# Performance work log

Hardware: AMD Instinct MI355X
Metric: run time of the kernel (lower is better)

Reference implementation:

```python
import jax, jax.numpy as jnp
import numpy as np

N, DZ, DQ = 65536, 128, 512


def setup_inputs() -> dict:
    key = jax.random.key(0)
    kz, kb, kg = jax.random.split(key, 3)
    z = jax.random.normal(kz, (N, DZ), dtype=jnp.float32)
    # match torch init scaling: beta ~ 0.01*randn, gamma ~ 0.05*randn
    beta = jax.random.normal(kb, (DQ, DZ), dtype=jnp.float32) * 0.01
    gamma = jax.random.normal(kg, (DQ, DZ), dtype=jnp.float32) * 0.05
    return {"z": z, "beta": beta, "gamma": gamma}


def reference(z, beta, gamma):
    # zero-inflated Poisson sampling decoder
    logits = jnp.einsum("nd,qd->nq", z, beta)          # [N, dq]
    pi = jax.nn.sigmoid(logits)                          # exp(x)/(1+exp(x))
    rate = jnp.nan_to_num(jnp.exp(jnp.einsum("nd,qd->nq", z, gamma)), nan=1e-4)
    rate = jnp.abs(rate) + 0.01
    key = jax.random.key(42)
    kp, kb = jax.random.split(key)
    poisson = jax.random.poisson(kp, rate).astype(jnp.float32)   # [N, dq]
    masking = jax.random.bernoulli(kb, 1.0 - pi).astype(jnp.float32)
    return masking * poisson
```

## Files before the change

### kernel.cpp

```cpp
#include <hip/hip_runtime.h>
#include <stdint.h>

#pragma clang fp contract(off)

#define HALF_ 16777216u

#define WS_TSLOT 386
#define WS_RCNT  388
#define WS_P1E5  392
#define TBL_OFF_B 4096
#define TBL_K0 95904
#define TBL_N  8193
#define RWL_OFF_B   81920
#define RWLCAP 16384u
#define PCNT_OFF_B  212992
#define KCNT_OFF_B  475136
#define BTT_OFF_B   786432
#define GTT_OFF_B   1048576
#define DYN2_OFF_B  1310720
#define PCAP_BLK 128u
#define KCAP_BLK 128u
#define NBLK 65536u
#define P1WL_OFF_B  DYN2_OFF_B
#define KWL_OFF_B   (DYN2_OFF_B + 33554432u)
#define NEED_V4     (KWL_OFF_B + 33554432u)
#define V2WL_OFF_B 40960
#define V2WLCAP 16384u
#define V2BT_OFF_B 172032

__device__ __forceinline__ void tf2x32(uint32_t k0, uint32_t k1,
                                       uint32_t x0, uint32_t x1,
                                       uint32_t& o0, uint32_t& o1) {
  uint32_t ks2 = k0 ^ k1 ^ 0x1BD11BDAu;
  x0 += k0; x1 += k1;
#define TFR(r) x0 += x1; x1 = (x1 << (r)) | (x1 >> (32 - (r))); x1 ^= x0;
  TFR(13) TFR(15) TFR(26) TFR(6)
  x0 += k1;  x1 += ks2 + 1u;
  TFR(17) TFR(29) TFR(16) TFR(24)
  x0 += ks2; x1 += k0 + 2u;
  TFR(13) TFR(15) TFR(26) TFR(6)
  x0 += k0;  x1 += k1 + 3u;
  TFR(17) TFR(29) TFR(16) TFR(24)
  x0 += k1;  x1 += ks2 + 4u;
  TFR(13) TFR(15) TFR(26) TFR(6)
  x0 += ks2; x1 += k0 + 5u;
#undef TFR
  o0 = x0; o1 = x1;
}

__device__ __forceinline__ uint32_t tfx(uint32_t k0, uint32_t k1, uint32_t i) {
  uint32_t o0, o1;
  tf2x32(k0, k1, 0u, i, o0, o1);
  return o0 ^ o1;
}

__device__ __forceinline__ float u01(uint32_t bits) {
  return __uint_as_float((bits >> 9) | 0x3f800000u) - 1.0f;
}

__device__ __forceinline__ float csqrt(float x) {
  return (float)__builtin_sqrt((double)x);
}

__device__ __forceinline__ float eexp(float xin) {
  float c = fminf(xin, 88.3762626647950f);
  c = fmaxf(c, -88.3762626647949f);
  float fx = floorf(__builtin_fmaf(c, 1.44269504088896341f, 0.5f));
  float x = __builtin_fmaf(-0.693359375f, fx, c);
  x = __builtin_fmaf(2.12194440e-4f, fx, x);
  float z = x * x;
  float y = __builtin_fmaf(x, 1.9875691500e-4f, 1.3981999507e-3f);
  y = __builtin_fmaf(y, x, 8.3334519073e-3f);
  y = __builtin_fmaf(y, x, 4.1665795894e-2f);
  y = __builtin_fmaf(y, x, 1.6666665459e-1f);
  y = __builtin_fmaf(y, x, 5.0000001201e-1f);
  y = __builtin_fmaf(y, z, x);
  y = 1.0f + y;
  int e = (int)fx;
  float s = __uint_as_float((uint32_t)(e + 127) << 23);
  return fmaxf(y * s, xin);
}

__device__ __forceinline__ float elog(float xin) {
  float x = fmaxf(xin, 1.17549435e-38f);
  uint32_t bits = __float_as_uint(x);
  float e = (float)((int)(bits >> 23) - 0x7e);
  x = __uint_as_float((bits & 0x807fffffu) | 0x3f000000u);
  bool mask = x < 0.707106781186547524f;
  float tmp = mask ? x : 0.0f;
  x = x - 1.0f;
  e = e - (mask ? 1.0f : 0.0f);
  x = x + tmp;
  float z = x * x;
  float y = __builtin_fmaf(7.0376836292e-2f, x, -1.1514610310e-1f);
  y = __builtin_fmaf(y, x, 1.1676998740e-1f);
  y = __builtin_fmaf(y, x, -1.2420140846e-1f);
  y = __builtin_fmaf(y, x, 1.4249322787e-1f);
  y = __builtin_fmaf(y, x, -1.6668057665e-1f);
  y = __builtin_fmaf(y, x, 2.0000714765e-1f);
  y = __builtin_fmaf(y, x, -2.4999993993e-1f);
  y = __builtin_fmaf(y, x, 3.3333331174e-1f);
  y = y * x;
  y = y * z;
  y = __builtin_fmaf(e, -2.12194440e-4f, y);
  y = __builtin_fmaf(-0.5f, z, y);
  x = x + y;
  x = __builtin_fmaf(e, 0.693359375f, x);
  if (xin == 0.0f) x = -__builtin_inff();
  return x;
}

__device__ __forceinline__ float xlog1p(float x) {
  float small_ = __builtin_fmaf(-0.5f, x, 1.0f) * x;
  float large_ = elog(x + 1.0f);
  return (fabsf(x) < 1e-4f) ? small_ : large_;
}

__device__ __forceinline__ float xlgamma(float input) {
  float z = input - 1.0f;
  float x = 0.99999999999980993227684700473478f;
  const float lcs[8] = {
      676.520368121885098567009190444019f,
      -1259.13921672240287047156078755283f,
      771.3234287776530788486528258894f,
      -176.61502916214059906584551354f,
      12.507343278686904814458936853f,
      -0.13857109526572011689554707f,
      9.984369578019570859563e-6f,
      1.50563273514931155834e-7f};
#pragma unroll
  for (int i = 0; i < 8; ++i) {
    x = x + lcs[i] / ((z + (float)i) + 1.0f);
  }
  float t = 7.5f + z;
  float log_t = 2.0149030205422647f + xlog1p(z / 7.5f);
  float log_y = __builtin_fmaf((z + 0.5f) - t / log_t, log_t,
                               0.91893853320467274178f) + elog(x);
  return log_y;
}

struct TrsP { float ll, bb, aa, ia, vr; };
__device__ __forceinline__ TrsP trs_params(float lam) {
  TrsP p;
  p.ll = elog(lam);
  p.bb = __builtin_fmaf(2.53f, csqrt(lam), 0.931f);
  p.aa = __builtin_fmaf(0.02483f, p.bb, -0.059f);
  p.ia = 1.1239f + 1.1328f / (p.bb - 3.4f);
  p.vr = 0.9277f - 3.6224f / (p.bb - 2.0f);
  return p;
}

__device__ __forceinline__ bool trs_step(float lam, const TrsP& p,
                                         float u, float v, float& kout) {
  float us = 0.5f - fabsf(u);
  float t2 = (2.0f * p.aa) / us + p.bb;
  float k = floorf(__builtin_fmaf(t2, u, lam) + 0.43f);
  kout = k;
  bool accept1 = (us >= 0.07f) && (v <= p.vr);
  if (accept1) return true;
  bool reject = (k < 0.0f) || ((us < 0.013f) && (v > us));
  if (reject) return false;
  float s = elog(v * p.ia / (p.aa / (us * us) + p.bb));
  float tt = __builtin_fmaf(k, p.ll, -lam) - xlgamma(k + 1.0f);
  return s <= tt;
}

__global__ void chain_v2(uint32_t* __restrict__ ws) {
  int lane = threadIdx.x;
  uint32_t kpa = 0, kpb = 0;
  if (lane == 0) {
    uint32_t a0, b0;
    tf2x32(0u, 42u, 0u, 0u, kpa, kpb);
    tf2x32(0u, 42u, 0u, 1u, a0, b0);
    ws[0] = a0; ws[1] = b0;
  }
  kpa = __shfl(kpa, 0); kpb = __shfl(kpb, 0);
  uint32_t kra = kpa, krb = kpb;
  uint32_t kja = kpa, kjb = kpb;
  for (int i = 0; i < 64; ++i) {
    bool isrej = (lane >= 2 && lane <= 4);
    uint32_t key0 = isrej ? kja : kra;
    uint32_t key1 = isrej ? kjb : krb;
    uint32_t xx = (lane == 1) ? 1u : (lane == 3) ? 1u : (lane == 4) ? 2u : 0u;
    uint32_t o0, o1;
    tf2x32(key0, key1, 0u, xx, o0, o1);
    if (lane == 1) { ws[2 + 2 * i] = o0; ws[3 + 2 * i] = o1; }
    if (lane == 3) { ws[130 + 4 * i] = o0; ws[131 + 4 * i] = o1; }
    if (lane == 4) { ws[132 + 4 * i] = o0; ws[133 + 4 * i] = o1; }
    kra = __shfl(o0, 0); krb = __shfl(o1, 0);
    kja = __shfl(o0, 2); kjb = __shfl(o1, 2);
  }
  if (lane == 0) {
    TrsP p = trs_params(1e5f);
    float* wf = (float*)(ws + WS_P1E5);
    wf[0] = p.ll; wf[1] = p.bb; wf[2] = p.aa; wf[3] = p.ia; wf[4] = p.vr;
    ws[WS_TSLOT] = 0u;
    ws[WS_RCNT] = 0u;
  }
}

__global__ __launch_bounds__(256) void lgt_kernel(uint32_t* __restrict__ ws) {
  int j = blockIdx.x * 256 + threadIdx.x;
  if (j >= TBL_N) return;
  float* tbl = (float*)((char*)ws + TBL_OFF_B);
  tbl[j] = xlgamma((float)(TBL_K0 + j) + 1.0f);
}

__global__ __launch_bounds__(256) void transpose_kernel(
    const float* __restrict__ b, const float* __restrict__ g,
    float* __restrict__ bT, float* __restrict__ gT) {
  int i = blockIdx.x * 256 + threadIdx.x;
  int q = i >> 7, d = i & 127;
  bT[d * 512 + q] = b[i];
  gT[d * 512 + q] = g[i];
}

__global__ __launch_bounds__(256) void transpose_tiled(
    const float* __restrict__ b, const float* __restrict__ g,
    float* __restrict__ bTT, float* __restrict__ gTT) {
  int i = blockIdx.x * 256 + threadIdx.x;
  int q = i >> 7, d = i & 127;
  int dst = (d >> 2) * 2048 + (q << 2) + (d & 3);
  bTT[dst] = b[i];
  gTT[dst] = g[i];
}

struct P1C { float ll, bb, aa, ia, vr; };

__device__ __forceinline__ bool p1_eval(const P1C& c, const float* __restrict__ tbl,
                                        uint32_t s00, uint32_t s01,
                                        uint32_t s10, uint32_t s11, uint32_t idx) {
  float u = u01(tfx(s00, s01, idx)) - 0.5f;
  float v = u01(tfx(s10, s11, idx));
  float us = 0.5f - fabsf(u);
  if (us >= 0.07f && v <= c.vr) return true;
  float t2 = (2.0f * c.aa) / us + c.bb;
  float k = floorf(__builtin_fmaf(t2, u, 1e5f) + 0.43f);
  if ((k < 0.0f) || ((us < 0.013f) && (v > us))) return false;
  float arg = v * c.ia / (c.aa / (us * us) + c.bb);
  int ki = (int)k - TBL_K0;
  float lg = (ki >= 0 && ki < TBL_N) ? tbl[ki] : xlgamma(k + 1.0f);
  float tt = __builtin_fmaf(k, c.ll, -1e5f) - lg;
  float sf = __logf(arg);
  if (sf <= tt - 1e-4f) return true;
  if (sf > tt + 1e-4f) return false;
  return elog(arg) <= tt;
}

__device__ uint32_t p1_scan(const P1C& c, const float* __restrict__ tbl,
                            const uint32_t* __restrict__ rej, uint32_t idx) {
  for (int it = 1; it < 64; ++it) {
    if (p1_eval(c, tbl, rej[4 * it], rej[4 * it + 1], rej[4 * it + 2],
                rej[4 * it + 3], idx))
      return (uint32_t)it;
  }
  return 63u;
}

__global__ __launch_bounds__(256) void p1a_v4(
    uint32_t* ws, uint32_t* __restrict__ p1wl, uint32_t* __restrict__ pcnt) {
  __shared__ uint32_t ldsc;
  if (threadIdx.x == 0) ldsc = 0;
  __syncthreads();
  const float* wf = (const float*)(ws + WS_P1E5);
  P1C c{wf[0], wf[1], wf[2], wf[3], wf[4]};
  const float* tbl = (const float*)((const char*)ws + TBL_OFF_B);
  const uint32_t* rej = ws + 130;
  uint32_t s00 = rej[0], s01 = rej[1], s10 = rej[2], s11 = rej[3];
  uint32_t t = blockIdx.x * 256u + threadIdx.x;
  uint32_t* region = p1wl + blockIdx.x * PCAP_BLK;
  bool fa = !p1_eval(c, tbl, s00, s01, s10, s11, t);
  bool fb = !p1_eval(c, tbl, s00, s01, s10, s11, t + HALF_);
  if (fa) {
    uint32_t slot = atomicAdd(&ldsc, 1u);
    if (slot < PCAP_BLK) region[slot] = t;
    else atomicMax(ws + WS_TSLOT, p1_scan(c, tbl, rej, t));
  }
  if (fb) {
    uint32_t slot = atomicAdd(&ldsc, 1u);
    if (slot < PCAP_BLK) region[slot] = t + HALF_;
    else atomicMax(ws + WS_TSLOT, p1_scan(c, tbl, rej, t + HALF_));
  }
  __syncthreads();
  if (threadIdx.x == 0) pcnt[blockIdx.x] = ldsc;
}

__global__ __launch_bounds__(256) void p1b_v4(
    uint32_t* ws, const uint32_t* __restrict__ p1wl,
    const uint32_t* __restrict__ pcnt) {
  const float* wf = (const float*)(ws + WS_P1E5);
  P1C c{wf[0], wf[1], wf[2], wf[3], wf[4]};
  const float* tbl = (const float*)((const char*)ws + TBL_OFF_B);
  const uint32_t* rej = ws + 130;
  uint32_t fmax = 0;
  uint32_t total = NBLK * PCAP_BLK;
  for (uint32_t s = blockIdx.x * 256u + threadIdx.x; s < total;
       s += gridDim.x * 256u) {
    uint32_t b = s >> 7, i = s & (PCAP_BLK - 1u);
    uint32_t cnt = pcnt[b];
    if (cnt > PCAP_BLK) cnt = PCAP_BLK;
    if (i < cnt) {
      uint32_t f = p1_scan(c, tbl, rej, p1wl[s]);
      if (f > fmax) fmax = f;
    }
  }
  for (int off = 32; off > 0; off >>= 1) {
    uint32_t o = __shfl_down(fmax, off, 64);
    if (o > fmax) fmax = o;
  }
  if ((threadIdx.x & 63) == 0 && fmax > 0) atomicMax(ws + WS_TSLOT, fmax);
}

__device__ __forceinline__ int first_accept_exact(float lam, uint32_t idx,
                                                  const uint32_t* __restrict__ rej) {
  TrsP p = trs_params(lam);
  for (int it = 0; it < 64; ++it) {
    float u = u01(tfx(rej[4 * it + 0], rej[4 * it + 1], idx)) - 0.5f;
    float v = u01(tfx(rej[4 * it + 2], rej[4 * it + 3], idx));
    float kk;
    if (trs_step(lam, p, u, v, kk)) return it;
  }
  return 63;
}

__device__ float knuth_finish(float lp, float lam, bool fD, bool m,
                              const uint32_t* __restrict__ wsk, uint32_t idx) {
  const float del = 4e-6f * (lam + 4.0f);
  int k = 4;
  bool fU = false;
  for (int it = 4; it < 64; ++it) {
    float d = lp + lam;
    bool nb = fabsf(d) < del;
    if (d > 0.0f) {
      fD = nb; k++;
      lp = lp + __logf(u01(tfx(wsk[2 * it], wsk[2 * it + 1], idx)));
    } else { fU = nb; break; }
  }
  float p = (float)(k - 1);
  float ph = p + ((fD && fU) ? 0.0f : (fD ? -0.5f : (fU ? 0.5f : 0.0f)));
  return m ? ph : 0.0f;
}

__global__ __launch_bounds__(256) void zip_v4(
    const float* __restrict__ z, uint32_t* ws,
    uint32_t* __restrict__ kwl, uint32_t* __restrict__ kcnt,
    float* __restrict__ out) {
  __shared__ uint32_t ldsc;
  if (threadIdx.x == 0) ldsc = 0;
  __syncthreads();
  uint32_t t = blockIdx.x * 256u + threadIdx.x;
  uint32_t n = t >> 9, q = t & 511u, n2 = n + 32768u;

  const float4* z4a = (const float4*)(z + (size_t)n * 128u);
  const float4* z4b = (const float4*)(z + (size_t)n2 * 128u);
  const float4* bt4 = (const float4*)((const char*)ws + BTT_OFF_B);
  const float4* gt4 = (const float4*)((const char*)ws + GTT_OFF_B);

  float lA = 0.f, lB = 0.f, gA = 0.f, gB = 0.f;
  for (int d4 = 0; d4 < 32; ++d4) {
    float4 bv = bt4[(d4 << 9) + q];
    float4 gv = gt4[(d4 << 9) + q];
    float4 z1 = z4a[d4], z2 = z4b[d4];
    lA = lA + z1.x * bv.x; lB = lB + z2.x * bv.x; gA = gA + z1.x * gv.x; gB = gB + z2.x * gv.x;
    lA = lA + z1.y * bv.y; lB = lB + z2.y * bv.y; gA = gA + z1.y * gv.y; gB = gB + z2.y * gv.y;
    lA = lA + z1.z * bv.z; lB = lB + z2.z * bv.z; gA = gA + z1.z * gv.z; gB = gB + z2.z * gv.z;
    lA = lA + z1.w * bv.w; lB = lB + z2.w * bv.w; gA = gA + z1.w * gv.w; gB = gB + z2.w * gv.w;
  }

  float piA = 1.0f / (1.0f + eexp(-lA));
  float piB = 1.0f / (1.0f + eexp(-lB));
  float lamA = fabsf(eexp(gA)) + 0.01f;
  float lamB = fabsf(eexp(gB)) + 0.01f;

  float dmA = u01(tfx(ws[0], ws[1], t)) - (1.0f - piA);
  float dmB = u01(tfx(ws[0], ws[1], t + HALF_)) - (1.0f - piB);
  bool mA = dmA < 0.0f, mB = dmB < 0.0f;
  bool mfA = fabsf(dmA) < 2e-6f, mfB = fabsf(dmB) < 2e-6f;

  bool knuA = lamA < 10.0f, knuB = lamB < 10.0f;

  const uint32_t* wsk = ws + 2;
  const float delA = 4e-6f * (lamA + 4.0f);
  const float delB = 4e-6f * (lamB + 4.0f);
  float lpA = 0.f, lpB = 0.f;
  int kA = 0, kB = 0;
  bool goA = knuA, goB = knuB;
  bool fDA = false, fUA = false, fDB = false, fUB = false;
#pragma unroll
  for (int it = 0; it < 4; ++it) {
    uint32_t w0 = wsk[2 * it], w1 = wsk[2 * it + 1];
    if (goA) {
      float d = lpA + lamA;
      bool nb = fabsf(d) < delA;
      if (d > 0.0f) { fDA = nb; kA++; lpA = lpA + __logf(u01(tfx(w0, w1, t))); }
      else          { fUA = nb; goA = false; }
    }
    if (goB) {
      float d = lpB + lamB;
      bool nb = fabsf(d) < delB;
      if (d > 0.0f) { fDB = nb; kB++; lpB = lpB + __logf(u01(tfx(w0, w1, t + HALF_))); }
      else          { fUB = nb; goB = false; }
    }
  }
  bool survA = knuA && goA, survB = knuB && goB;

  const uint32_t* rejk = ws + 130;
  uint32_t* rwl = (uint32_t*)((char*)ws + RWL_OFF_B);
  if (!knuA) {
    atomicMax(ws + WS_TSLOT, (uint32_t)first_accept_exact(lamA, t, rejk));
    uint32_t slot = atomicAdd(ws + WS_RCNT, 1u);
    if (slot < RWLCAP) {
      rwl[2 * slot] = t | (mA ? 0x80000000u : 0u);
      rwl[2 * slot + 1] = __float_as_uint(lamA);
    }
  }
  if (!knuB) {
    atomicMax(ws + WS_TSLOT, (uint32_t)first_accept_exact(lamB, t + HALF_, rejk));
    uint32_t slot = atomicAdd(ws + WS_RCNT, 1u);
    if (slot < RWLCAP) {
      rwl[2 * slot] = (t + HALF_) | (mB ? 0x80000000u : 0u);
      rwl[2 * slot + 1] = __float_as_uint(lamB);
    }
  }

  uint32_t* region = kwl + blockIdx.x * KCAP_BLK;
  if (survA) {
    uint32_t slot = atomicAdd(&ldsc, 1u);
    if (slot < KCAP_BLK) region[slot] = t | ((uint32_t)mA << 25);
    else out[t] = knuth_finish(lpA, lamA, fDA, mA, wsk, t);
  } else if (knuA) {
    float pA = (float)(kA - 1);
    float hiA = pA + (fUA ? 0.5f : 0.0f);
    float resA;
    if (mfA && hiA <= 1.2f) resA = 0.5f * hiA;
    else {
      float ph = pA + ((fDA && fUA) ? 0.0f : (fDA ? -0.5f : (fUA ? 0.5f : 0.0f)));
      resA = mA ? ph : 0.0f;
    }
    out[t] = resA;
  } else {
    out[t] = 0.0f;
  }

  if (survB) {
    uint32_t slot = atomicAdd(&ldsc, 1u);
    if (slot < KCAP_BLK) region[slot] = (t + HALF_) | ((uint32_t)mB << 25);
    else out[t + HALF_] = knuth_finish(lpB, lamB, fDB, mB, wsk, t + HALF_);
  } else if (knuB) {
    float pB = (float)(kB - 1);
    float hiB = pB + (fUB ? 0.5f : 0.0f);
    float resB;
    if (mfB && hiB <= 1.2f) resB = 0.5f * hiB;
    else {
      float ph = pB + ((fDB && fUB) ? 0.0f : (fDB ? -0.5f : (fUB ? 0.5f : 0.0f)));
      resB = mB ? ph : 0.0f;
    }
    out[t + HALF_] = resB;
  } else {
    out[t + HALF_] = 0.0f;
  }
  __syncthreads();
  if (threadIdx.x == 0) kcnt[blockIdx.x] = ldsc;
}

__global__ __launch_bounds__(256) void k3b_v4(
    uint32_t* ws, const float* __restrict__ z,
    const uint32_t* __restrict__ kwl, const uint32_t* __restrict__ kcnt,
    float* __restrict__ out) {
  const uint32_t* wsk = ws + 2;
  const float4* gt4 = (const float4*)((const char*)ws + GTT_OFF_B);
  uint32_t total = NBLK * KCAP_BLK;
  for (uint32_t s = blockIdx.x * 256u + threadIdx.x; s < total;
       s += gridDim.x * 256u) {
    uint32_t b = s >> 7, i = s & (KCAP_BLK - 1u);
    uint32_t cnt = kcnt[b];
    if (cnt > KCAP_BLK) cnt = KCAP_BLK;
    if (i >= cnt) continue;
    uint32_t w = kwl[s];
    uint32_t idx = w & 0x01FFFFFFu;
    bool m = (w >> 25) & 1u;
    uint32_t n = idx >> 9, q = idx & 511u;
    const float4* z4 = (const float4*)(z + (size_t)n * 128u);
    float g = 0.f;
    for (int d4 = 0; d4 < 32; ++d4) {
      float4 gv = gt4[(d4 << 9) + q];
      float4 z1 = z4[d4];
      g = g + z1.x * gv.x;
      g = g + z1.y * gv.y;
      g = g + z1.z * gv.z;
      g = g + z1.w * gv.w;
    }
    float lam = fabsf(eexp(g)) + 0.01f;
    const float del = 4e-6f * (lam + 4.0f);
    float lp = 0.f;
    bool fD = false;
#pragma unroll
    for (int it = 0; it < 4; ++it) {
      float d = lp + lam;
      fD = fabsf(d) < del;
      lp = lp + __logf(u01(tfx(wsk[2 * it], wsk[2 * it + 1], idx)));
    }
    out[idx] = knuth_finish(lp, lam, fD, m, wsk, idx);
  }
}

__global__ __launch_bounds__(256) void k3_kernel(
    const uint32_t* ws, const uint32_t* __restrict__ wl, uint32_t cap,
    float* __restrict__ out) {
  uint32_t cnt = ws[WS_RCNT];
  if (cnt > cap) cnt = cap;
  uint32_t Traw = ws[WS_TSLOT];
  int Tmax = (int)(Traw > 63u ? 63u : Traw);
  const uint32_t* rej = ws + 130;
  for (uint32_t i = blockIdx.x * 256u + threadIdx.x; i < cnt;
       i += gridDim.x * 256u) {
    uint32_t im = wl[2 * i];
    float lam = __uint_as_float(wl[2 * i + 1]);
    uint32_t idx = im & 0x7FFFFFFFu;
    bool mask = (im >> 31) != 0u;
    TrsP p = trs_params(lam);
    float klast = -1.0f;
    for (int it = 0; it <= Tmax; ++it) {
      float u = u01(tfx(rej[4 * it + 0], rej[4 * it + 1], idx)) - 0.5f;
      float v = u01(tfx(rej[4 * it + 2], rej[4 * it + 3], idx));
      float kk;
      if (trs_step(lam, p, u, v, kk)) klast = kk;
    }
    out[idx] = mask ? klast : 0.0f;
  }
}


__global__ __launch_bounds__(256) void pass1_lite(
    const uint32_t* __restrict__ chain, uint32_t* __restrict__ Tslot) {
  const float* wf = (const float*)(chain + WS_P1E5);
  P1C c{wf[0], wf[1], wf[2], wf[3], wf[4]};
  const float* tbl = (const float*)((const char*)chain + TBL_OFF_B);
  uint32_t t = blockIdx.x * 256u + threadIdx.x;
  const uint32_t* rej = chain + 130;
  int faA = 63, faB = 63;
  bool accA = false, accB = false;
  for (int it = 0; it < 64; ++it) {
    if (accA && accB) break;
    uint32_t s00 = rej[4 * it + 0], s01 = rej[4 * it + 1];
    uint32_t s10 = rej[4 * it + 2], s11 = rej[4 * it + 3];
    if (!accA && p1_eval(c, tbl, s00, s01, s10, s11, t)) { accA = true; faA = it; }
    if (!accB && p1_eval(c, tbl, s00, s01, s10, s11, t + HALF_)) { accB = true; faB = it; }
  }
  int fa = faA > faB ? faA : faB;
  for (int off = 32; off > 0; off >>= 1) {
    int o = __shfl_down(fa, off, 64);
    fa = fa > o ? fa : o;
  }
  __shared__ int smax[4];
  int wave = threadIdx.x >> 6, lanei = threadIdx.x & 63;
  if (lanei == 0) smax[wave] = fa;
  __syncthreads();
  if (threadIdx.x == 0) {
    int m01 = smax[0] > smax[1] ? smax[0] : smax[1];
    int m23 = smax[2] > smax[3] ? smax[2] : smax[3];
    int m = m01 > m23 ? m01 : m23;
    atomicMax(Tslot, (uint32_t)m);
  }
}

__global__ __launch_bounds__(256) void zip_v2(
    const float* __restrict__ z, const float* __restrict__ bT,
    const float* __restrict__ gT, uint32_t* ws, float* __restrict__ out) {
  uint32_t t = blockIdx.x * 256u + threadIdx.x;
  uint32_t n = t >> 9, q = t & 511u, n2 = n + 32768u;
  const float* zr  = z + (size_t)n * 128u;
  const float* zr2 = z + (size_t)n2 * 128u;
  float lA = 0.f, lB = 0.f, gA = 0.f, gB = 0.f;
  for (int d = 0; d < 128; ++d) {
    float bv = bT[d * 512 + q];
    float gv = gT[d * 512 + q];
    float z1 = zr[d], z2 = zr2[d];
    lA = lA + z1 * bv;
    lB = lB + z2 * bv;
    gA = gA + z1 * gv;
    gB = gB + z2 * gv;
  }
  float piA = 1.0f / (1.0f + eexp(-lA));
  float piB = 1.0f / (1.0f + eexp(-lB));
  float lamA = fabsf(eexp(gA)) + 0.01f;
  float lamB = fabsf(eexp(gB)) + 0.01f;
  bool knuA = lamA < 10.0f, knuB = lamB < 10.0f;
  float pA = 0.f, pB = 0.f;
  bool fDA = false, fUA = false, fDB = false, fUB = false;
  {
    const uint32_t* wsk = ws + 2;
    const float delA = 4e-6f * (lamA + 4.0f);
    const float delB = 4e-6f * (lamB + 4.0f);
    float lpA = 0.f, lpB = 0.f;
    int kA = 0, kB = 0;
    bool goA = knuA, goB = knuB;
    for (int it = 0; it < 64; ++it) {
      if (!goA && !goB) break;
      uint32_t w0 = wsk[2 * it], w1 = wsk[2 * it + 1];
      if (goA) {
        float d = lpA + lamA;
        bool nb = fabsf(d) < delA;
        if (d > 0.0f) { fDA = nb; kA++; lpA = lpA + __logf(u01(tfx(w0, w1, t))); }
        else          { fUA = nb; goA = false; }
      }
      if (goB) {
        float d = lpB + lamB;
        bool nb = fabsf(d) < delB;
        if (d > 0.0f) { fDB = nb; kB++; lpB = lpB + __logf(u01(tfx(w0, w1, t + HALF_))); }
        else          { fUB = nb; goB = false; }
      }
    }
    if (knuA) pA = (float)(kA - 1);
    if (knuB) pB = (float)(kB - 1);
  }
  float dmA = u01(tfx(ws[0], ws[1], t)) - (1.0f - piA);
  float dmB = u01(tfx(ws[0], ws[1], t + HALF_)) - (1.0f - piB);
  bool mA = dmA < 0.0f, mB = dmB < 0.0f;
  bool mfA = fabsf(dmA) < 2e-6f, mfB = fabsf(dmB) < 2e-6f;
  uint32_t* wl = (uint32_t*)((char*)ws + V2WL_OFF_B);
  const uint32_t* rejk = ws + 130;
  float resA, resB;
  if (!knuA) {
    atomicMax(ws + WS_TSLOT, (uint32_t)first_accept_exact(lamA, t, rejk));
    uint32_t slot = atomicAdd(ws + WS_RCNT, 1u);
    if (slot < V2WLCAP) {
      wl[2 * slot] = t | (mA ? 0x80000000u : 0u);
      wl[2 * slot + 1] = __float_as_uint(lamA);
    }
    resA = 0.0f;
  } else {
    float hiA = pA + (fUA ? 0.5f : 0.0f);
    if (mfA && hiA <= 1.2f) resA = 0.5f * hiA;
    else {
      float ph = pA + ((fDA && fUA) ? 0.0f : (fDA ? -0.5f : (fUA ? 0.5f : 0.0f)));
      resA = mA ? ph : 0.0f;
    }
  }
  if (!knuB) {
    atomicMax(ws + WS_TSLOT, (uint32_t)first_accept_exact(lamB, t + HALF_, rejk));
    uint32_t slot = atomicAdd(ws + WS_RCNT, 1u);
    if (slot < V2WLCAP) {
      wl[2 * slot] = (t + HALF_) | (mB ? 0x80000000u : 0u);
      wl[2 * slot + 1] = __float_as_uint(lamB);
    }
    resB = 0.0f;
  } else {
    float hiB = pB + (fUB ? 0.5f : 0.0f);
    if (mfB && hiB <= 1.2f) resB = 0.5f * hiB;
    else {
      float ph = pB + ((fDB && fUB) ? 0.0f : (fDB ? -0.5f : (fUB ? 0.5f : 0.0f)));
      resB = mB ? ph : 0.0f;
    }
  }
  out[t] = resA;
  out[t + HALF_] = resB;
}

extern "C" void kernel_launch(void* const* d_in, const int* in_sizes, int n_in,
                              void* d_out, int out_size, void* d_ws, size_t ws_size,
                              hipStream_t stream) {
  const float* z     = (const float*)d_in[0];
  const float* beta  = (const float*)d_in[1];
  const float* gamma = (const float*)d_in[2];
  float* out = (float*)d_out;
  uint32_t* ws = (uint32_t*)d_ws;

  if (ws_size >= NEED_V4) {
    float* bTT = (float*)((char*)d_ws + BTT_OFF_B);
    float* gTT = (float*)((char*)d_ws + GTT_OFF_B);
    uint32_t* p1wl = (uint32_t*)((char*)d_ws + P1WL_OFF_B);
    uint32_t* kwl  = (uint32_t*)((char*)d_ws + KWL_OFF_B);
    uint32_t* pcnt = (uint32_t*)((char*)d_ws + PCNT_OFF_B);
    uint32_t* kcnt = (uint32_t*)((char*)d_ws + KCNT_OFF_B);
    uint32_t* rwl  = (uint32_t*)((char*)d_ws + RWL_OFF_B);

    chain_v2<<<1, 64, 0, stream>>>(ws);
    lgt_kernel<<<(TBL_N + 255) / 256, 256, 0, stream>>>(ws);
    transpose_tiled<<<256, 256, 0, stream>>>(beta, gamma, bTT, gTT);
    p1a_v4<<<NBLK, 256, 0, stream>>>(ws, p1wl, pcnt);
    p1b_v4<<<2048, 256, 0, stream>>>(ws, p1wl, pcnt);
    zip_v4<<<NBLK, 256, 0, stream>>>(z, ws, kwl, kcnt, out);
    k3b_v4<<<2048, 256, 0, stream>>>(ws, z, kwl, kcnt, out);
    k3_kernel<<<64, 256, 0, stream>>>(ws, rwl, RWLCAP, out);
  } else {
    float* bT = (float*)((char*)d_ws + V2BT_OFF_B);
    float* gT = bT + 512 * 128;
    uint32_t* rwl = (uint32_t*)((char*)d_ws + V2WL_OFF_B);
    chain_v2<<<1, 64, 0, stream>>>(ws);
    lgt_kernel<<<(TBL_N + 255) / 256, 256, 0, stream>>>(ws);
    transpose_kernel<<<256, 256, 0, stream>>>(beta, gamma, bT, gT);
    pass1_lite<<<HALF_ / 256u, 256, 0, stream>>>(ws, ws + WS_TSLOT);
    zip_v2<<<HALF_ / 256u, 256, 0, stream>>>(z, bT, gT, ws, out);
    k3_kernel<<<64, 256, 0, stream>>>(ws, rwl, V2WLCAP, out);
  }
}
```

Baseline: 1.592 ms.

## Fuse pass-1 rejection eval into zip kernel and interleave beta/gamma for packed FMA

Drops the separate p1a pass over all 2×16M elements and runs the pass-1 rejection check inside zip_v5, only for elements on the Knuth path (knuA/knuB). This removes one full-grid launch and its recomputation. Beta and gamma are interleaved into a single layout so the two dot products can use packed v2f multiply-adds. The change also reorders the schedule so p1b now runs after zip. k3b reads gamma out of the interleaved buffer, loading twice the bytes it needs. It relies on the p1 worklist only being consumed later by k3_kernel, so correctness depends on that ordering.

```diff
diff --git a/kernel.cpp b/kernel.cpp
--- a/kernel.cpp
+++ b/kernel.cpp
@@ -4,6 +4,8 @@
 #pragma clang fp contract(off)
 
 #define HALF_ 16777216u
+
+typedef float v2f __attribute__((ext_vector_type(2)));
 
 #define WS_TSLOT 386
 #define WS_RCNT  388
@@ -15,15 +17,14 @@
 #define RWLCAP 16384u
 #define PCNT_OFF_B  212992
 #define KCNT_OFF_B  475136
-#define BTT_OFF_B   786432
-#define GTT_OFF_B   1048576
+#define BG_OFF_B    786432
 #define DYN2_OFF_B  1310720
 #define PCAP_BLK 128u
 #define KCAP_BLK 128u
 #define NBLK 65536u
 #define P1WL_OFF_B  DYN2_OFF_B
 #define KWL_OFF_B   (DYN2_OFF_B + 33554432u)
-#define NEED_V4     (KWL_OFF_B + 33554432u)
+#define NEED_V5     (KWL_OFF_B + 33554432u)
 #define V2WL_OFF_B 40960
 #define V2WLCAP 16384u
 #define V2BT_OFF_B 172032
@@ -215,14 +216,14 @@
   gT[d * 512 + q] = g[i];
 }
 
-__global__ __launch_bounds__(256) void transpose_tiled(
+__global__ __launch_bounds__(256) void transpose_bg(
     const float* __restrict__ b, const float* __restrict__ g,
-    float* __restrict__ bTT, float* __restrict__ gTT) {
+    float* __restrict__ bg) {
   int i = blockIdx.x * 256 + threadIdx.x;
   int q = i >> 7, d = i & 127;
-  int dst = (d >> 2) * 2048 + (q << 2) + (d & 3);
-  bTT[dst] = b[i];
-  gTT[dst] = g[i];
+  int base = ((d >> 1) * 512 + q) * 4 + (d & 1) * 2;
+  bg[base] = b[i];
+  bg[base + 1] = g[i];
 }
 
 struct P1C { float ll, bb, aa, ia, vr; };
@@ -257,34 +258,6 @@
   return 63u;
 }
 
-__global__ __launch_bounds__(256) void p1a_v4(
-    uint32_t* ws, uint32_t* __restrict__ p1wl, uint32_t* __restrict__ pcnt) {
-  __shared__ uint32_t ldsc;
-  if (threadIdx.x == 0) ldsc = 0;
-  __syncthreads();
-  const float* wf = (const float*)(ws + WS_P1E5);
-  P1C c{wf[0], wf[1], wf[2], wf[3], wf[4]};
-  const float* tbl = (const float*)((const char*)ws + TBL_OFF_B);
-  const uint32_t* rej = ws + 130;
-  uint32_t s00 = rej[0], s01 = rej[1], s10 = rej[2], s11 = rej[3];
-  uint32_t t = blockIdx.x * 256u + threadIdx.x;
-  uint32_t* region = p1wl + blockIdx.x * PCAP_BLK;
-  bool fa = !p1_eval(c, tbl, s00, s01, s10, s11, t);
-  bool fb = !p1_eval(c, tbl, s00, s01, s10, s11, t + HALF_);
-  if (fa) {
-    uint32_t slot = atomicAdd(&ldsc, 1u);
-    if (slot < PCAP_BLK) region[slot] = t;
-    else atomicMax(ws + WS_TSLOT, p1_scan(c, tbl, rej, t));
-  }
-  if (fb) {
-    uint32_t slot = atomicAdd(&ldsc, 1u);
-    if (slot < PCAP_BLK) region[slot] = t + HALF_;
-    else atomicMax(ws + WS_TSLOT, p1_scan(c, tbl, rej, t + HALF_));
-  }
-  __syncthreads();
-  if (threadIdx.x == 0) pcnt[blockIdx.x] = ldsc;
-}
-
 __global__ __launch_bounds__(256) void p1b_v4(
     uint32_t* ws, const uint32_t* __restrict__ p1wl,
     const uint32_t* __restrict__ pcnt) {
@@ -341,31 +314,38 @@
   return m ? ph : 0.0f;
 }
 
-__global__ __launch_bounds__(256) void zip_v4(
+__global__ __launch_bounds__(256) void zip_v5(
     const float* __restrict__ z, uint32_t* ws,
     uint32_t* __restrict__ kwl, uint32_t* __restrict__ kcnt,
+    uint32_t* __restrict__ p1wl, uint32_t* __restrict__ pcnt,
     float* __restrict__ out) {
-  __shared__ uint32_t ldsc;
-  if (threadIdx.x == 0) ldsc = 0;
+  __shared__ uint32_t ldsk, ldsp;
+  if (threadIdx.x == 0) { ldsk = 0; ldsp = 0; }
   __syncthreads();
   uint32_t t = blockIdx.x * 256u + threadIdx.x;
   uint32_t n = t >> 9, q = t & 511u, n2 = n + 32768u;
 
   const float4* z4a = (const float4*)(z + (size_t)n * 128u);
   const float4* z4b = (const float4*)(z + (size_t)n2 * 128u);
-  const float4* bt4 = (const float4*)((const char*)ws + BTT_OFF_B);
-  const float4* gt4 = (const float4*)((const char*)ws + GTT_OFF_B);
-
-  float lA = 0.f, lB = 0.f, gA = 0.f, gB = 0.f;
+  const float4* bg4 = (const float4*)((const char*)ws + BG_OFF_B);
+
+  v2f accA = {0.f, 0.f}, accB = {0.f, 0.f};
   for (int d4 = 0; d4 < 32; ++d4) {
-    float4 bv = bt4[(d4 << 9) + q];
-    float4 gv = gt4[(d4 << 9) + q];
     float4 z1 = z4a[d4], z2 = z4b[d4];
-    lA = lA + z1.x * bv.x; lB = lB + z2.x * bv.x; gA = gA + z1.x * gv.x; gB = gB + z2.x * gv.x;
-    lA = lA + z1.y * bv.y; lB = lB + z2.y * bv.y; gA = gA + z1.y * gv.y; gB = gB + z2.y * gv.y;
-    lA = lA + z1.z * bv.z; lB = lB + z2.z * bv.z; gA = gA + z1.z * gv.z; gB = gB + z2.z * gv.z;
-    lA = lA + z1.w * bv.w; lB = lB + z2.w * bv.w; gA = gA + z1.w * gv.w; gB = gB + z2.w * gv.w;
-  }
+    float4 p01 = bg4[(d4 * 2 + 0) * 512 + q];
+    float4 p23 = bg4[(d4 * 2 + 1) * 512 + q];
+    v2f bg0 = {p01.x, p01.y}, bg1 = {p01.z, p01.w};
+    v2f bg2v = {p23.x, p23.y}, bg3 = {p23.z, p23.w};
+    accA = accA + bg0 * (v2f){z1.x, z1.x};
+    accB = accB + bg0 * (v2f){z2.x, z2.x};
+    accA = accA + bg1 * (v2f){z1.y, z1.y};
+    accB = accB + bg1 * (v2f){z2.y, z2.y};
+    accA = accA + bg2v * (v2f){z1.z, z1.z};
+    accB = accB + bg2v * (v2f){z2.z, z2.z};
+    accA = accA + bg3 * (v2f){z1.w, z1.w};
+    accB = accB + bg3 * (v2f){z2.w, z2.w};
+  }
+  float lA = accA.x, gA = accA.y, lB = accB.x, gB = accB.y;
 
   float piA = 1.0f / (1.0f + eexp(-lA));
   float piB = 1.0f / (1.0f + eexp(-lB));
@@ -404,6 +384,25 @@
   }
   bool survA = knuA && goA, survB = knuB && goB;
 
+  {
+    const float* wf = (const float*)(ws + WS_P1E5);
+    P1C c{wf[0], wf[1], wf[2], wf[3], wf[4]};
+    const float* tbl = (const float*)((const char*)ws + TBL_OFF_B);
+    const uint32_t* rej = ws + 130;
+    uint32_t s00 = rej[0], s01 = rej[1], s10 = rej[2], s11 = rej[3];
+    uint32_t* pregion = p1wl + blockIdx.x * PCAP_BLK;
+    if (knuA && !p1_eval(c, tbl, s00, s01, s10, s11, t)) {
+      uint32_t slot = atomicAdd(&ldsp, 1u);
+      if (slot < PCAP_BLK) pregion[slot] = t;
+      else atomicMax(ws + WS_TSLOT, p1_scan(c, tbl, rej, t));
+    }
+    if (knuB && !p1_eval(c, tbl, s00, s01, s10, s11, t + HALF_)) {
+      uint32_t slot = atomicAdd(&ldsp, 1u);
+      if (slot < PCAP_BLK) pregion[slot] = t + HALF_;
+      else atomicMax(ws + WS_TSLOT, p1_scan(c, tbl, rej, t + HALF_));
+    }
+  }
+
   const uint32_t* rejk = ws + 130;
   uint32_t* rwl = (uint32_t*)((char*)ws + RWL_OFF_B);
   if (!knuA) {
@@ -425,7 +424,7 @@
 
   uint32_t* region = kwl + blockIdx.x * KCAP_BLK;
   if (survA) {
-    uint32_t slot = atomicAdd(&ldsc, 1u);
+    uint32_t slot = atomicAdd(&ldsk, 1u);
     if (slot < KCAP_BLK) region[slot] = t | ((uint32_t)mA << 25);
     else out[t] = knuth_finish(lpA, lamA, fDA, mA, wsk, t);
   } else if (knuA) {
@@ -443,7 +442,7 @@
   }
 
   if (survB) {
-    uint32_t slot = atomicAdd(&ldsc, 1u);
+    uint32_t slot = atomicAdd(&ldsk, 1u);
     if (slot < KCAP_BLK) region[slot] = (t + HALF_) | ((uint32_t)mB << 25);
     else out[t + HALF_] = knuth_finish(lpB, lamB, fDB, mB, wsk, t + HALF_);
   } else if (knuB) {
@@ -460,15 +459,15 @@
     out[t + HALF_] = 0.0f;
   }
   __syncthreads();
-  if (threadIdx.x == 0) kcnt[blockIdx.x] = ldsc;
-}
-
-__global__ __launch_bounds__(256) void k3b_v4(
+  if (threadIdx.x == 0) { kcnt[blockIdx.x] = ldsk; pcnt[blockIdx.x] = ldsp; }
+}
+
+__global__ __launch_bounds__(256) void k3b_v5(
     uint32_t* ws, const float* __restrict__ z,
     const uint32_t* __restrict__ kwl, const uint32_t* __restrict__ kcnt,
     float* __restrict__ out) {
   const uint32_t* wsk = ws + 2;
-  const float4* gt4 = (const float4*)((const char*)ws + GTT_OFF_B);
+  const float4* bg4 = (const float4*)((const char*)ws + BG_OFF_B);
   uint32_t total = NBLK * KCAP_BLK;
   for (uint32_t s = blockIdx.x * 256u + threadIdx.x; s < total;
        s += gridDim.x * 256u) {
@@ -483,12 +482,13 @@
     const float4* z4 = (const float4*)(z + (size_t)n * 128u);
     float g = 0.f;
     for (int d4 = 0; d4 < 32; ++d4) {
-      float4 gv = gt4[(d4 << 9) + q];
       float4 z1 = z4[d4];
-      g = g + z1.x * gv.x;
-      g = g + z1.y * gv.y;
-      g = g + z1.z * gv.z;
-      g = g + z1.w * gv.w;
+      float4 p01 = bg4[(d4 * 2 + 0) * 512 + q];
+      float4 p23 = bg4[(d4 * 2 + 1) * 512 + q];
+      g = g + p01.y * z1.x;
+      g = g + p01.w * z1.y;
+      g = g + p23.y * z1.z;
+      g = g + p23.w * z1.w;
     }
     float lam = fabsf(eexp(g)) + 0.01f;
     const float del = 4e-6f * (lam + 4.0f);
@@ -666,9 +666,8 @@
   float* out = (float*)d_out;
   uint32_t* ws = (uint32_t*)d_ws;
 
-  if (ws_size >= NEED_V4) {
-    float* bTT = (float*)((char*)d_ws + BTT_OFF_B);
-    float* gTT = (float*)((char*)d_ws + GTT_OFF_B);
+  if (ws_size >= NEED_V5) {
+    float* bg = (float*)((char*)d_ws + BG_OFF_B);
     uint32_t* p1wl = (uint32_t*)((char*)d_ws + P1WL_OFF_B);
     uint32_t* kwl  = (uint32_t*)((char*)d_ws + KWL_OFF_B);
     uint32_t* pcnt = (uint32_t*)((char*)d_ws + PCNT_OFF_B);
@@ -677,11 +676,10 @@
 
     chain_v2<<<1, 64, 0, stream>>>(ws);
     lgt_kernel<<<(TBL_N + 255) / 256, 256, 0, stream>>>(ws);
-    transpose_tiled<<<256, 256, 0, stream>>>(beta, gamma, bTT, gTT);
-    p1a_v4<<<NBLK, 256, 0, stream>>>(ws, p1wl, pcnt);
+    transpose_bg<<<256, 256, 0, stream>>>(beta, gamma, bg);
+    zip_v5<<<NBLK, 256, 0, stream>>>(z, ws, kwl, kcnt, p1wl, pcnt, out);
     p1b_v4<<<2048, 256, 0, stream>>>(ws, p1wl, pcnt);
-    zip_v4<<<NBLK, 256, 0, stream>>>(z, ws, kwl, kcnt, out);
-    k3b_v4<<<2048, 256, 0, stream>>>(ws, z, kwl, kcnt, out);
+    k3b_v5<<<2048, 256, 0, stream>>>(ws, z, kwl, kcnt, out);
     k3_kernel<<<64, 256, 0, stream>>>(ws, rwl, RWLCAP, out);
   } else {
     float* bT = (float*)((char*)d_ws + V2BT_OFF_B);
```

Result: slower. 1.924 ms (+20.8%).
